# Kernel tuning notes

Hardware: AMD Instinct MI355X
Metric: run time of the kernel (lower is better)

## Reference

```python
import jax, jax.numpy as jnp
import numpy as np
from jax import lax

BN_EPS = 1e-4  # both BatchNorm2d (epsilon=0.0001) and BatchNorm1d (eps=0.0001)


def bin_act(x):
    # deterministic 1-bit activation: 2*round(clamp((x+1)/2,0,1)) - 1
    return 2.0 * jnp.round(jnp.clip((x + 1.0) * 0.5, 0.0, 1.0)) - 1.0


def bin_w(w):
    # H = 1.0: wb = (round(clamp((w+1)/2,0,1))*2 - 1) * 1.0  -> values in {-1,+1}
    return 2.0 * jnp.round(jnp.clip((w + 1.0) * 0.5, 0.0, 1.0)) - 1.0


def conv3x3(x, w, b):
    # NCHW input, OIHW weight, stride 1, padding 1 (SAME for 3x3)
    y = lax.conv_general_dilated(x, bin_w(w), (1, 1), ((1, 1), (1, 1)),
                                 dimension_numbers=('NCHW', 'OIHW', 'NCHW'))
    return y + b[None, :, None, None]


def maxpool2(x):
    return lax.reduce_window(x, -jnp.inf, lax.max, (1, 1, 2, 2), (1, 1, 2, 2), 'VALID')


def bn2d(x, g, b):
    # training-mode BatchNorm2d: batch stats over (N,H,W), biased variance
    m = jnp.mean(x, axis=(0, 2, 3), keepdims=True)
    v = jnp.mean(jnp.square(x - m), axis=(0, 2, 3), keepdims=True)
    return (x - m) * lax.rsqrt(v + BN_EPS) * g[None, :, None, None] + b[None, :, None, None]


def bn1d(x, g, b):
    m = jnp.mean(x, axis=0)
    v = jnp.mean(jnp.square(x - m), axis=0)
    return (x - m) * lax.rsqrt(v + BN_EPS) * g + b


def linear(x, w, b):
    return x @ bin_w(w).T + b


def setup_inputs() -> dict:
    key = jax.random.key(0)
    ks = jax.random.split(key, 16)
    d = {}
    d['x'] = jax.random.normal(ks[0], (256, 3, 32, 32), jnp.float32)
    conv_shapes = [(128, 3), (128, 128), (256, 128), (256, 256), (512, 256), (512, 512)]
    for i, (co, ci) in enumerate(conv_shapes, start=1):
        d[f'cw{i}'] = jax.random.normal(ks[i], (co, ci, 3, 3), jnp.float32)
        d[f'cb{i}'] = jax.random.normal(jax.random.fold_in(ks[i], 1), (co,), jnp.float32) * 0.01
        d[f'g{i}'] = jnp.ones((co,), jnp.float32)
        d[f'be{i}'] = jnp.zeros((co,), jnp.float32)
    fc_shapes = [(1024, 8192), (1024, 1024), (10, 1024)]
    for i, (fo, fi) in enumerate(fc_shapes, start=1):
        d[f'fw{i}'] = jax.random.normal(ks[6 + i], (fo, fi), jnp.float32)
        d[f'fb{i}'] = jax.random.normal(jax.random.fold_in(ks[6 + i], 1), (fo,), jnp.float32) * 0.01
        d[f'gf{i}'] = jnp.ones((fo,), jnp.float32)
        d[f'bef{i}'] = jnp.zeros((fo,), jnp.float32)
    return d


def reference(x, cw1, cb1, g1, be1, cw2, cb2, g2, be2, cw3, cb3, g3, be3,
              cw4, cb4, g4, be4, cw5, cb5, g5, be5, cw6, cb6, g6, be6,
              fw1, fb1, gf1, bef1, fw2, fb2, gf2, bef2, fw3, fb3, gf3, bef3):
    x = bin_act(bn2d(conv3x3(x, cw1, cb1), g1, be1))                 # [B,128,32,32]
    x = bin_act(bn2d(maxpool2(conv3x3(x, cw2, cb2)), g2, be2))       # [B,128,16,16]
    x = bin_act(bn2d(conv3x3(x, cw3, cb3), g3, be3))                 # [B,256,16,16]
    x = bin_act(bn2d(maxpool2(conv3x3(x, cw4, cb4)), g4, be4))       # [B,256,8,8]
    x = bin_act(bn2d(conv3x3(x, cw5, cb5), g5, be5))                 # [B,512,8,8]
    x = bin_act(bn2d(maxpool2(conv3x3(x, cw6, cb6)), g6, be6))       # [B,512,4,4]
    x = x.reshape(x.shape[0], -1)                                     # [B,8192]
    x = bin_act(bn1d(linear(x, fw1, fb1), gf1, bef1))                 # [B,1024]
    x = bin_act(bn1d(linear(x, fw2, fb2), gf2, bef2))                 # [B,1024]
    x = bn1d(linear(x, fw3, fb3), gf3, bef3)                          # [B,10]
    return x
```

## Files before the change

kernel.cpp:

```cpp
#include <hip/hip_runtime.h>

using u64 = unsigned long long;


__device__ __forceinline__ int bin01(float x) {
  float u = (x + 1.0f) * 0.5f;
  u = fminf(fmaxf(u, 0.0f), 1.0f);
  return rintf(u) != 0.0f;
}

__global__ void pack_conv_w(const float* __restrict__ w, u64* __restrict__ out,
                            int Cout, int Cin) {
  const int cqn = Cin >> 6;
  const int total = Cout * 9 * cqn;
  const int idx = blockIdx.x * 256 + threadIdx.x;
  if (idx >= total) return;
  int r = idx;
  const int q = r % cqn; r /= cqn;
  const int kx = r % 3; r /= 3;
  const int ky = r % 3;
  const int co = r / 3;
  u64 word = 0;
  for (int l = 0; l < 64; ++l) {
    const int ci = q * 64 + l;
    if (bin01(w[((size_t)(co * Cin + ci) * 3 + ky) * 3 + kx])) word |= (1ull << l);
  }
  out[idx] = word;
}

__global__ void pack_corr(const u64* __restrict__ W, int* __restrict__ CT) {
  const int idx = blockIdx.x * 256 + threadIdx.x;
  const int b1 = 1152, b2 = 3456, b3 = 5760, b4 = 10368, b5 = 14976;
  if (idx >= b5) return;
  int lo, woff, cq;
  if (idx < b1)      { lo = 0;  woff = 0;     cq = 2; }
  else if (idx < b2) { lo = b1; woff = 2304;  cq = 2; }
  else if (idx < b3) { lo = b2; woff = 6912;  cq = 4; }
  else if (idx < b4) { lo = b3; woff = 16128; cq = 4; }
  else               { lo = b4; woff = 34560; cq = 8; }
  const int rel = idx - lo;
  const int co = rel / 9, p = rel % 9;
  const int r = p / 3, c = p % 3;
  int corr = 0;
  for (int dy = 0; dy < 3; ++dy)
    for (int dx = 0; dx < 3; ++dx) {
      const bool inv = (r == 1 && dy == 0) || (r == 2 && dy == 2) ||
                       (c == 1 && dx == 0) || (c == 2 && dx == 2);
      if (inv) {
        const u64* wp = W + woff + ((size_t)(co * 9 + dy * 3 + dx)) * cq;
        for (int q = 0; q < cq; ++q) corr += __popcll(wp[q]);
      }
    }
  CT[idx] = corr;
}

__global__ void pack_fc_w(const float* __restrict__ w, u64* __restrict__ out,
                          int Fi, int Fo) {
  const int fiq = Fi >> 6;
  const int total = Fo * fiq;
  const int idx = blockIdx.x * 256 + threadIdx.x;
  if (idx >= total) return;
  const int q = idx % fiq, o = idx / fiq;
  u64 word = 0;
  for (int l = 0; l < 64; ++l)
    if (bin01(w[(size_t)o * Fi + q * 64 + l])) word |= (1ull << l);
  out[idx] = word;
}

__global__ void pack_fc1_w(const float* __restrict__ w, u64* __restrict__ out) {
  const int o = blockIdx.x;
  const int t = threadIdx.x;
  __shared__ float ls[8192];
  const float* wr = w + (size_t)o * 8192;
  for (int i = t; i < 8192; i += 256) ls[i] = wr[i];
  __syncthreads();
  if (t < 128) {
    const int q = t, cq = q & 7, hw = q >> 3;
    u64 word = 0;
    for (int l = 0; l < 64; ++l) {
      const int f = (cq * 64 + l) * 16 + hw;
      if (bin01(ls[f])) word |= (1ull << l);
    }
    out[(size_t)o * 128 + q] = word;
  }
}

__global__ void pack_w1f(const float* __restrict__ w1, float* __restrict__ w1f) {
  const int i = blockIdx.x * 256 + threadIdx.x;
  if (i < 3456) w1f[i] = bin01(w1[i]) ? 1.0f : -1.0f;
}

__device__ __forceinline__ void stage_image(const float* __restrict__ x, int n,
                                            float* __restrict__ xs, int nthreads,
                                            int t) {
  for (int idx = t; idx < 3 * 34 * 34; idx += nthreads) {
    const int ci = idx / 1156, rem = idx % 1156;
    const int hy = rem / 34, wx = rem % 34;
    float v = 0.0f;
    if (hy >= 1 && hy <= 32 && wx >= 1 && wx <= 32)
      v = x[(size_t)n * 3072 + ci * 1024 + (hy - 1) * 32 + (wx - 1)];
    xs[idx] = v;
  }
}

template <int PASS>
__global__ void conv1_eval(const float* __restrict__ x,
                           const float* __restrict__ w1f,
                           const float* __restrict__ cb,
                           const float* __restrict__ st,
                           float* __restrict__ BL) {
  const int blk = blockIdx.x;
  const int n = blk >> 2, q = blk & 3;
  const int t = threadIdx.x;
  __shared__ float xs[3 * 34 * 34];
  __shared__ float yl[256 * 8];
  __shared__ float rl[2 * 8 * 8];
  stage_image(x, n, xs, 256, t);
  __syncthreads();
  const int hw = q * 256 + t;
  const int h = hw >> 5, w = hw & 31;
  float win[27];
#pragma unroll
  for (int k = 0; k < 27; ++k) {
    const int ci = k / 9, dy = (k % 9) / 3, dx = k % 3;
    win[k] = xs[ci * 1156 + (h + dy) * 34 + (w + dx)];
  }
  for (int cc = 0; cc < 16; ++cc) {
    float y8[8];
#pragma unroll
    for (int j8 = 0; j8 < 8; ++j8) {
      const int c = cc * 8 + j8;
      const float* wp = w1f + c * 27;
      float acc = 0.0f;
#pragma unroll
      for (int k = 0; k < 27; ++k) acc = fmaf(wp[k], win[k], acc);
      float y = acc + cb[c];
      if (PASS) { const float d = y - st[2 * c]; y = d * d; }
      y8[j8] = y;
    }
    __syncthreads();
#pragma unroll
    for (int j8 = 0; j8 < 8; ++j8) yl[t * 8 + j8] = y8[j8];
    __syncthreads();
    if (t < 128) {
      const int L = t >> 6, j = (t >> 3) & 7, c8 = t & 7;
      float r = yl[(L * 128 + j) * 8 + c8];
      for (int i = 1; i < 16; ++i) r += yl[(L * 128 + i * 8 + j) * 8 + c8];
      rl[(L * 8 + c8) * 8 + j] = r;
    }
    __syncthreads();
    if (t < 16) {
      const int L = t >> 3, c8 = t & 7;
      const float* p = rl + (L * 8 + c8) * 8;
      const float s =
          ((p[0] + p[1]) + (p[2] + p[3])) + ((p[4] + p[5]) + (p[6] + p[7]));
      BL[((size_t)(n * 8) + (q * 2 + L)) * 128 + (cc * 8 + c8)] = s;
    }
  }
}

__global__ void conv1_comb2(const float* __restrict__ BL, float* __restrict__ st,
                            int pass) {
  const int t = threadIdx.x;
  const int lane = t & 63;
  const int wid = t >> 6;
  const int c = blockIdx.x * 32 + wid * 8 + (lane & 7);
  const int leaf = lane >> 3;
  const float* base = BL + (size_t)leaf * 128 + c;
  float S = 0.0f;
#pragma unroll 4
  for (int n = 0; n < 256; ++n) {
    const float v = base[(size_t)n * 1024];
    const float a = v + __shfl_xor(v, 8);
    const float b = a + __shfl_xor(a, 16);
    const float Ln = b + __shfl_xor(b, 32);
    S = (n == 0) ? Ln : (S + Ln);
  }
  if (leaf == 0) {
    if (pass == 0) st[2 * c] = S / 262144.0f;
    else           st[2 * c + 1] = 1.0f / sqrtf(S / 262144.0f + 1e-4f);
  }
}

__global__ void conv1_binz(const float* __restrict__ x,
                           const float* __restrict__ w1f,
                           const float* __restrict__ cb,
                           const float* __restrict__ st,
                           const float* __restrict__ g,
                           const float* __restrict__ be,
                           u64* __restrict__ out) {
  const int blk = blockIdx.x;
  const int n = blk >> 2, q = blk & 3;
  const int t = threadIdx.x;
  __shared__ float xs[3 * 34 * 34];
  stage_image(x, n, xs, 256, t);
  __syncthreads();
  const int hw = q * 256 + t;
  const int h = hw >> 5, w = hw & 31;
  float win[27];
#pragma unroll
  for (int k = 0; k < 27; ++k) {
    const int ci = k / 9, dy = (k % 9) / 3, dx = k % 3;
    win[k] = xs[ci * 1156 + (h + dy) * 34 + (w + dx)];
  }
  u64 m0 = 0, m1 = 0;
  for (int c = 0; c < 128; ++c) {
    const float* wp = w1f + c * 27;
    float acc = 0.0f;
#pragma unroll
    for (int k = 0; k < 27; ++k) acc = fmaf(wp[k], win[k], acc);
    const float y = acc + cb[c];
    const float tv = ((y - st[2 * c]) * st[2 * c + 1]) * g[c] + be[c];
    const u64 bit = (u64)bin01(tv);
    if (c < 64) m0 |= bit << c;
    else        m1 |= bit << (c - 64);
  }
  u64* dst = out + ((size_t)(n * 1024 + hw)) * 2;
  dst[0] = m0;
  dst[1] = m1;
}

template <int CQ, int H>
__device__ __forceinline__ void zero_halo(u64* __restrict__ xs, int t) {
  constexpr int HP = H + 2;
  constexpr int HALO = 2 * HP * CQ + 2 * H * CQ;
  for (int j = t; j < HALO; j += 256) {
    int widx;
    if (j < HP * CQ) widx = j;
    else if (j < 2 * HP * CQ) widx = (H + 1) * HP * CQ + (j - HP * CQ);
    else {
      const int r = j - 2 * HP * CQ;
      const int row = (r / (2 * CQ)) + 1;
      const int s = r & (2 * CQ - 1);
      const int col = (s < CQ) ? 0 : (HP - 1);
      widx = (row * HP + col) * CQ + (s & (CQ - 1));
    }
    xs[widx] = 0;
  }
}

template <int CQ, int POOL, int H, int COUT, int NCPB>
__launch_bounds__(256, 3)
__global__ void conv_bin_halo(const u64* __restrict__ xin, const u64* __restrict__ wpk,
                              const int* __restrict__ ct, short* __restrict__ pre) {
  constexpr int OH = H / POOL;
  constexpr int PLANE = OH * OH;
  constexpr int G = 256 / PLANE;
  constexpr int NE = POOL * POOL;
  constexpr int HP = H + 2;
  constexpr int NWP = HP * HP * CQ;
  constexpr int QC = (CQ > 4) ? 4 : CQ;
  constexpr int NQC = CQ / QC;
  constexpr int IW = H * H * CQ;
  constexpr int VEC = IW / 256;
  const int n = blockIdx.x;
  const int t = threadIdx.x;
  __shared__ __align__(16) u64 xs[NWP];
  const u64* src = xin + (size_t)n * IW;
  {
    const int i0 = t * VEC;
    const int q0 = i0 & (CQ - 1);
    const int w0 = (i0 / CQ) & (H - 1);
    const int h0 = i0 / (CQ * H);
    const int dst0 = ((h0 + 1) * HP + (w0 + 1)) * CQ + q0;
    if constexpr (VEC >= 2) {
      ulonglong2 tmp[VEC / 2];
#pragma unroll
      for (int v = 0; v < VEC / 2; ++v)
        tmp[v] = *reinterpret_cast<const ulonglong2*>(&src[i0 + 2 * v]);
      zero_halo<CQ, H>(xs, t);
#pragma unroll
      for (int v = 0; v < VEC / 2; ++v)
        *reinterpret_cast<ulonglong2*>(&xs[dst0 + 2 * v]) = tmp[v];
    } else {
      const u64 tv = src[i0];
      zero_halo<CQ, H>(xs, t);
      xs[dst0] = tv;
    }
  }
  __syncthreads();
  int cosub;
  if constexpr (PLANE >= 64) cosub = __builtin_amdgcn_readfirstlane(t / PLANE);
  else cosub = t / PLANE;
  const int pos = t % PLANE;
  const int oh = pos / OH, ow = pos % OH;

  int cbase[NE];
#pragma unroll
  for (int py = 0; py < POOL; ++py)
#pragma unroll
    for (int px = 0; px < POOL; ++px)
      cbase[py * POOL + px] = ((oh * POOL + py) * HP + (ow * POOL + px)) * CQ;

  int pc[NCPB][NE];
#pragma unroll
  for (int cc = 0; cc < NCPB; ++cc)
#pragma unroll
    for (int e = 0; e < NE; ++e) pc[cc][e] = 0;

#pragma unroll
  for (int qc = 0; qc < NQC; ++qc) {
#pragma unroll
    for (int k = 0; k < 9; ++k) {
      const int dy = k / 3, dx = k % 3;
      const int koff = (dy * HP + dx) * CQ + qc * QC;
      u64 cw[NE][QC];
#pragma unroll
      for (int e = 0; e < NE; ++e) {
        const u64* cp = &xs[cbase[e] + koff];
#pragma unroll
        for (int q = 0; q < QC; ++q) cw[e][q] = cp[q];
      }
#pragma unroll
      for (int cc = 0; cc < NCPB; ++cc) {
        const int co = (blockIdx.y * NCPB + cc) * G + cosub;
        const u64* wp = wpk + ((size_t)co * 9 + k) * CQ + qc * QC;
        u64 w[QC];
#pragma unroll
        for (int q = 0; q < QC; ++q) w[q] = wp[q];
#pragma unroll
        for (int e = 0; e < NE; ++e) {
          int acc = pc[cc][e];
#pragma unroll
          for (int q = 0; q < QC; ++q) acc += __popcll(cw[e][q] ^ w[q]);
          pc[cc][e] = acc;
        }
      }
    }
  }

  int vcnt[NE];
#pragma unroll
  for (int py = 0; py < POOL; ++py) {
#pragma unroll
    for (int px = 0; px < POOL; ++px) {
      int cvn = 0;
#pragma unroll
      for (int dy = 0; dy < 3; ++dy)
#pragma unroll
        for (int dx = 0; dx < 3; ++dx) {
          const int hh = oh * POOL + py + dy - 1, ww = ow * POOL + px + dx - 1;
          cvn += (((unsigned)hh < (unsigned)H) && ((unsigned)ww < (unsigned)H)) ? 1 : 0;
        }
      vcnt[py * POOL + px] = cvn;
    }
  }
  int cofs[NE];
#pragma unroll
  for (int py = 0; py < POOL; ++py)
#pragma unroll
    for (int px = 0; px < POOL; ++px) {
      const int chh = oh * POOL + py, cww = ow * POOL + px;
      const int rr = (chh == 0) ? 1 : ((chh == H - 1) ? 2 : 0);
      const int cl = (cww == 0) ? 1 : ((cww == H - 1) ? 2 : 0);
      cofs[py * POOL + px] = rr * 3 + cl;
    }
#pragma unroll
  for (int cc = 0; cc < NCPB; ++cc) {
    const int co = (blockIdx.y * NCPB + cc) * G + cosub;
    const int* ctp = ct + co * 9;
    int best = -1000000;
#pragma unroll
    for (int e = 0; e < NE; ++e) {
      const int dot = vcnt[e] * (CQ * 64) - 2 * (pc[cc][e] - ctp[cofs[e]]);
      best = dot > best ? dot : best;
    }
    pre[((size_t)(n * COUT + co) * OH + oh) * OH + ow] = (short)best;
  }
}

template <int CQ, int POOL, int H, int COUT, int NCPB>
__launch_bounds__(256, 4)
__global__ void conv_bin_pred(const u64* __restrict__ xin, const u64* __restrict__ wpk,
                              short* __restrict__ pre) {
  constexpr int OH = H / POOL;
  constexpr int PLANE = OH * OH;
  constexpr int G = 256 / PLANE;
  constexpr int NE = POOL * POOL;
  constexpr int NW_ = H * H * CQ;
  constexpr int QC = (CQ > 4) ? 4 : CQ;
  constexpr int NQC = CQ / QC;
  const int n = blockIdx.x;
  const int t = threadIdx.x;
  __shared__ u64 xs[NW_];
  const u64* src = xin + (size_t)n * NW_;
  for (int i = t; i < NW_; i += 256) xs[i] = src[i];
  __syncthreads();
  const int cosub = t / PLANE;
  const int pos = t % PLANE;
  const int oh = pos / OH, ow = pos % OH;

  int pc[NCPB][NE];
#pragma unroll
  for (int cc = 0; cc < NCPB; ++cc)
#pragma unroll
    for (int e = 0; e < NE; ++e) pc[cc][e] = 0;

#pragma unroll
  for (int qc = 0; qc < NQC; ++qc) {
#pragma unroll
    for (int k = 0; k < 9; ++k) {
      const int dy = k / 3, dx = k % 3;
      u64 cw[NE][QC];
      bool cv[NE];
#pragma unroll
      for (int py = 0; py < POOL; ++py) {
#pragma unroll
        for (int px = 0; px < POOL; ++px) {
          const int hh = oh * POOL + py + dy - 1;
          const int ww = ow * POOL + px + dx - 1;
          const bool v = ((unsigned)hh < (unsigned)H) && ((unsigned)ww < (unsigned)H);
          const int e = py * POOL + px;
          cv[e] = v;
          const int base = v ? ((hh * H + ww) * CQ + qc * QC) : 0;
#pragma unroll
          for (int q = 0; q < QC; ++q) cw[e][q] = xs[base + q];
        }
      }
#pragma unroll
      for (int cc = 0; cc < NCPB; ++cc) {
        const int co = (blockIdx.y * NCPB + cc) * G + cosub;
        const u64* wp = wpk + ((size_t)co * 9 + k) * CQ + qc * QC;
        u64 w[QC];
#pragma unroll
        for (int q = 0; q < QC; ++q) w[q] = wp[q];
#pragma unroll
        for (int e = 0; e < NE; ++e) {
          int tp = 0;
#pragma unroll
          for (int q = 0; q < QC; ++q) tp += __popcll(cw[e][q] ^ w[q]);
          pc[cc][e] += cv[e] ? tp : 0;
        }
      }
    }
  }

  int vcnt[NE];
#pragma unroll
  for (int py = 0; py < POOL; ++py) {
#pragma unroll
    for (int px = 0; px < POOL; ++px) {
      int cvn = 0;
#pragma unroll
      for (int dy = 0; dy < 3; ++dy)
#pragma unroll
        for (int dx = 0; dx < 3; ++dx) {
          const int hh = oh * POOL + py + dy - 1, ww = ow * POOL + px + dx - 1;
          cvn += (((unsigned)hh < (unsigned)H) && ((unsigned)ww < (unsigned)H)) ? 1 : 0;
        }
      vcnt[py * POOL + px] = cvn;
    }
  }
#pragma unroll
  for (int cc = 0; cc < NCPB; ++cc) {
    const int co = (blockIdx.y * NCPB + cc) * G + cosub;
    int best = -1000000;
#pragma unroll
    for (int e = 0; e < NE; ++e) {
      const int dot = vcnt[e] * (CQ * 64) - 2 * pc[cc][e];
      best = dot > best ? dot : best;
    }
    pre[((size_t)(n * COUT + co) * OH + oh) * OH + ow] = (short)best;
  }
}

template <int PASS>
__device__ __forceinline__ float acc8(const short* __restrict__ p, float b, float m,
                                      int start, int len) {
  float r[8];
#pragma unroll
  for (int j = 0; j < 8; ++j) {
    float y = (float)p[start + j] + b;
    if (PASS) { const float d = y - m; y = d * d; }
    r[j] = y;
  }
  for (int i = 8; i < len; i += 8) {
#pragma unroll
    for (int j = 0; j < 8; ++j) {
      float y = (float)p[start + i + j] + b;
      if (PASS) { const float d = y - m; y = d * d; }
      r[j] += y;
    }
  }
  return ((r[0] + r[1]) + (r[2] + r[3])) + ((r[4] + r[5]) + (r[6] + r[7]));
}

template <int PASS>
__device__ __forceinline__ float np_sum_hw(const short* __restrict__ p, float b,
                                           float m, int HW) {
  if (HW == 256) return acc8<PASS>(p, b, m, 0, 128) + acc8<PASS>(p, b, m, 128, 128);
  return acc8<PASS>(p, b, m, 0, HW);
}

template <int HW>
__global__ void conv_stats(const short* __restrict__ pre, const float* __restrict__ cb,
                           float* __restrict__ st, int Cout) {
  const int c = blockIdx.x;
  const int n = threadIdx.x;
  const float b = cb[c];
  const short* p = pre + ((size_t)n * Cout + c) * HW;
  __shared__ float ls[256];
  ls[n] = np_sum_hw<0>(p, b, 0.0f, HW);
  __syncthreads();
  __shared__ float ms;
  if (n == 0) {
    float S = ls[0];
    for (int i = 1; i < 256; ++i) S += ls[i];
    ms = S / (float)(256 * HW);
  }
  __syncthreads();
  const float m = ms;
  __syncthreads();
  ls[n] = np_sum_hw<1>(p, b, m, HW);
  __syncthreads();
  if (n == 0) {
    float S = ls[0];
    for (int i = 1; i < 256; ++i) S += ls[i];
    const float v = S / (float)(256 * HW);
    st[2 * c] = m;
    st[2 * c + 1] = 1.0f / sqrtf(v + 1e-4f);
  }
}

__global__ void bin2d(const short* __restrict__ pre, const float* __restrict__ st,
                      const float* __restrict__ cb, const float* __restrict__ g,
                      const float* __restrict__ be, u64* __restrict__ out,
                      int Cout, int OH) {
  const int CQ = Cout >> 6;
  const int HW = OH * OH;
  const int widx = blockIdx.x * 256 + threadIdx.x;
  const int hw = widx % HW;
  const int r = widx / HW;
  const int cq = r % CQ;
  const int n = r / CQ;
  const short* p = pre + ((size_t)(n * Cout + cq * 64)) * HW + hw;
  u64 mask = 0;
  for (int c = 0; c < 64; ++c) {
    const int ch = cq * 64 + c;
    const float val = (float)p[(size_t)c * HW] + cb[ch];
    const float tv = ((val - st[2 * ch]) * st[2 * ch + 1]) * g[ch] + be[ch];
    mask |= ((u64)bin01(tv)) << c;
  }
  out[((size_t)n * HW + hw) * CQ + cq] = mask;
}

__global__ void transpose_act(const u64* __restrict__ a, u64* __restrict__ at) {
  const int widx = blockIdx.x * 256 + threadIdx.x;
  const int n = widx >> 7, q = widx & 127;
  at[(size_t)q * 256 + n] = a[widx];
}

__global__ void fc_layer_t(const u64* __restrict__ at, const u64* __restrict__ wpk,
                           short* __restrict__ pre) {
  const int o = blockIdx.x;
  const int n = threadIdx.x;
  const u64* wp = wpk + (size_t)o * 128;
  int pc = 0;
#pragma unroll 8
  for (int q = 0; q < 128; ++q) pc += __popcll(at[(size_t)q * 256 + n] ^ wp[q]);
  pre[(size_t)n * 1024 + o] = (short)(8192 - 2 * pc);
}

__global__ void fc_layer(const u64* __restrict__ xin, const u64* __restrict__ wpk,
                         short* __restrict__ pre, int FiQ, int Fo) {
  const int o = blockIdx.x;
  const int n = threadIdx.x;
  const u64* xp = xin + (size_t)n * FiQ;
  const u64* wp = wpk + (size_t)o * FiQ;
  int pc = 0;
  for (int q = 0; q < FiQ; ++q) pc += __popcll(xp[q] ^ wp[q]);
  pre[(size_t)n * Fo + o] = (short)(FiQ * 64 - 2 * pc);
}

__global__ void fc_stats(const short* __restrict__ pre, const float* __restrict__ fb,
                         float* __restrict__ st, int Fo) {
  const int o = blockIdx.x * blockDim.x + threadIdx.x;
  if (o >= Fo) return;
  const float b = fb[o];
  float S = (float)pre[o] + b;
#pragma unroll 8
  for (int n = 1; n < 256; ++n) S += (float)pre[(size_t)n * Fo + o] + b;
  const float m = S / 256.0f;
  float d0 = (float)pre[o] + b - m;
  float V = d0 * d0;
#pragma unroll 8
  for (int n = 1; n < 256; ++n) {
    const float d = (float)pre[(size_t)n * Fo + o] + b - m;
    V += d * d;
  }
  st[2 * o] = m;
  st[2 * o + 1] = 1.0f / sqrtf(V / 256.0f + 1e-4f);
}

__global__ void fc_bin(const short* __restrict__ pre, const float* __restrict__ st,
                       const float* __restrict__ fb, const float* __restrict__ g,
                       const float* __restrict__ be, u64* __restrict__ out, int Fo) {
  const int gid = blockIdx.x * 4 + (threadIdx.x >> 6);
  const int lane = threadIdx.x & 63;
  const int OQ = Fo >> 6;
  const int oq = gid % OQ, n = gid / OQ;
  const int o = oq * 64 + lane;
  const float val = (float)pre[(size_t)n * Fo + o] + fb[o];
  const float tv = ((val - st[2 * o]) * st[2 * o + 1]) * g[o] + be[o];
  const u64 mask = __ballot(bin01(tv));
  if (lane == 0) out[(size_t)n * OQ + oq] = mask;
}

__global__ void fc_out(const short* __restrict__ pre, const float* __restrict__ st,
                       const float* __restrict__ fb, const float* __restrict__ g,
                       const float* __restrict__ be, float* __restrict__ out) {
  const int i = blockIdx.x * 256 + threadIdx.x;
  if (i >= 2560) return;
  const int o = i % 10;
  const float val = (float)pre[i] + fb[o];
  out[i] = ((val - st[2 * o]) * st[2 * o + 1]) * g[o] + be[o];
}

extern "C" void kernel_launch(void* const* d_in, const int* in_sizes, int n_in,
                              void* d_out, int out_size, void* d_ws, size_t ws_size,
                              hipStream_t stream) {
  if (n_in < 37) return;
  const float* x = (const float*)d_in[0];
  const float *cw1 = (const float*)d_in[1],  *cb1 = (const float*)d_in[2],  *g1 = (const float*)d_in[3],  *be1 = (const float*)d_in[4];
  const float *cw2 = (const float*)d_in[5],  *cb2 = (const float*)d_in[6],  *g2 = (const float*)d_in[7],  *be2 = (const float*)d_in[8];
  const float *cw3 = (const float*)d_in[9],  *cb3 = (const float*)d_in[10], *g3 = (const float*)d_in[11], *be3 = (const float*)d_in[12];
  const float *cw4 = (const float*)d_in[13], *cb4 = (const float*)d_in[14], *g4 = (const float*)d_in[15], *be4 = (const float*)d_in[16];
  const float *cw5 = (const float*)d_in[17], *cb5 = (const float*)d_in[18], *g5 = (const float*)d_in[19], *be5 = (const float*)d_in[20];
  const float *cw6 = (const float*)d_in[21], *cb6 = (const float*)d_in[22], *g6 = (const float*)d_in[23], *be6 = (const float*)d_in[24];
  const float *fw1 = (const float*)d_in[25], *fb1 = (const float*)d_in[26], *gf1 = (const float*)d_in[27], *bef1 = (const float*)d_in[28];
  const float *fw2 = (const float*)d_in[29], *fb2 = (const float*)d_in[30], *gf2 = (const float*)d_in[31], *bef2 = (const float*)d_in[32];
  const float *fw3 = (const float*)d_in[33], *fb3 = (const float*)d_in[34], *gf3 = (const float*)d_in[35], *bef3 = (const float*)d_in[36];
  float* out = (float*)d_out;

  char* ws = (char*)d_ws;
  if (ws_size < 46137344) return;
  float* ST = (float*)ws;
  float* W1F = (float*)(ws + 32768);
  float* BL = (float*)(ws + 65536);
  u64* W = (u64*)(ws + 1179648);
  u64* A = (u64*)(ws + 2981888);
  int* CT = (int*)(ws + 12222464);
  short* PRE = (short*)(ws + 12582912);
  u64* AT6 = (u64*)(ws + 33554432);
  const int S1 = 0, S2 = 256, S3 = 512, S4 = 1024, S5 = 1536, S6 = 2560;
  const int SF1 = 3584, SF2 = 5632, SF3 = 7680;
  const size_t WC2 = 0, WC3 = 2304, WC4 = 6912, WC5 = 16128, WC6 = 34560;
  const size_t WF1 = 71424, WF2 = 202496, WF3 = 218880;
  const size_t A1 = 0, A2 = 524288, A3 = 655360, A4 = 917504, A5 = 983040;
  const size_t A6 = 1114112, AF1 = 1146880, AF2 = 1150976;
  const int CT2 = 0, CT3 = 1152, CT4 = 3456, CT5 = 5760;

  pack_w1f<<<14, 256, 0, stream>>>(cw1, W1F);
  pack_conv_w<<<9, 256, 0, stream>>>(cw2, W + WC2, 128, 128);
  pack_conv_w<<<18, 256, 0, stream>>>(cw3, W + WC3, 256, 128);
  pack_conv_w<<<36, 256, 0, stream>>>(cw4, W + WC4, 256, 256);
  pack_conv_w<<<72, 256, 0, stream>>>(cw5, W + WC5, 512, 256);
  pack_conv_w<<<144, 256, 0, stream>>>(cw6, W + WC6, 512, 512);
  pack_corr<<<59, 256, 0, stream>>>(W, CT);
  pack_fc1_w<<<1024, 256, 0, stream>>>(fw1, W + WF1);
  pack_fc_w<<<64, 256, 0, stream>>>(fw2, W + WF2, 1024, 1024);
  pack_fc_w<<<1, 256, 0, stream>>>(fw3, W + WF3, 1024, 10);

  conv1_eval<0><<<1024, 256, 0, stream>>>(x, W1F, cb1, ST + S1, BL);
  conv1_comb2<<<4, 256, 0, stream>>>(BL, ST + S1, 0);
  conv1_eval<1><<<1024, 256, 0, stream>>>(x, W1F, cb1, ST + S1, BL);
  conv1_comb2<<<4, 256, 0, stream>>>(BL, ST + S1, 1);
  conv1_binz<<<1024, 256, 0, stream>>>(x, W1F, cb1, ST + S1, g1, be1, A + A1);

  conv_bin_halo<2, 2, 32, 128, 8><<<dim3(256, 16), 256, 0, stream>>>(A + A1, W + WC2, CT + CT2, PRE);
  conv_stats<256><<<128, 256, 0, stream>>>(PRE, cb2, ST + S2, 128);
  bin2d<<<512, 256, 0, stream>>>(PRE, ST + S2, cb2, g2, be2, A + A2, 128, 16);

  conv_bin_halo<2, 1, 16, 256, 8><<<dim3(256, 32), 256, 0, stream>>>(A + A2, W + WC3, CT + CT3, PRE);
  conv_stats<256><<<256, 256, 0, stream>>>(PRE, cb3, ST + S3, 256);
  bin2d<<<1024, 256, 0, stream>>>(PRE, ST + S3, cb3, g3, be3, A + A3, 256, 16);

  conv_bin_halo<4, 2, 16, 256, 4><<<dim3(256, 16), 256, 0, stream>>>(A + A3, W + WC4, CT + CT4, PRE);
  conv_stats<64><<<256, 256, 0, stream>>>(PRE, cb4, ST + S4, 256);
  bin2d<<<256, 256, 0, stream>>>(PRE, ST + S4, cb4, g4, be4, A + A4, 256, 8);

  conv_bin_halo<4, 1, 8, 512, 8><<<dim3(256, 16), 256, 0, stream>>>(A + A4, W + WC5, CT + CT5, PRE);
  conv_stats<64><<<512, 256, 0, stream>>>(PRE, cb5, ST + S5, 512);
  bin2d<<<512, 256, 0, stream>>>(PRE, ST + S5, cb5, g5, be5, A + A5, 512, 8);

  conv_bin_pred<8, 2, 8, 512, 4><<<dim3(256, 8), 256, 0, stream>>>(A + A5, W + WC6, PRE);
  conv_stats<16><<<512, 256, 0, stream>>>(PRE, cb6, ST + S6, 512);
  bin2d<<<128, 256, 0, stream>>>(PRE, ST + S6, cb6, g6, be6, A + A6, 512, 4);

  transpose_act<<<128, 256, 0, stream>>>(A + A6, AT6);
  fc_layer_t<<<1024, 256, 0, stream>>>(AT6, W + WF1, PRE);
  fc_stats<<<16, 64, 0, stream>>>(PRE, fb1, ST + SF1, 1024);
  fc_bin<<<1024, 256, 0, stream>>>(PRE, ST + SF1, fb1, gf1, bef1, A + AF1, 1024);

  fc_layer<<<1024, 256, 0, stream>>>(A + AF1, W + WF2, PRE, 16, 1024);
  fc_stats<<<16, 64, 0, stream>>>(PRE, fb2, ST + SF2, 1024);
  fc_bin<<<1024, 256, 0, stream>>>(PRE, ST + SF2, fb2, gf2, bef2, A + AF2, 1024);

  fc_layer<<<10, 256, 0, stream>>>(A + AF2, W + WF3, PRE, 16, 10);
  fc_stats<<<1, 64, 0, stream>>>(PRE, fb3, ST + SF3, 10);
  fc_out<<<10, 256, 0, stream>>>(PRE, ST + SF3, fb3, gf3, bef3, out);
}
```

Before: 1.070 ms.

## Stage conv weights in LDS for packing, vectorize loads, fuse final FC layer

Conv weight packing now uses one block per output channel. Each block stages that channel's weights into shared memory with float4 loads and packs from there, instead of each thread doing strided global reads. The fc1 packing staging loop and the BN stats accumulation also switch to vectorized loads (float4 and 8-wide short). The last FC layer, its batch stats and its output normalization are merged into one single-block kernel, removing two launches. In exchange, the fused kernel computes its stats with only 10 threads in a serial loop, and the vector loads assume suitable alignment.

```diff
diff --git a/kernel.cpp b/kernel.cpp
--- a/kernel.cpp
+++ b/kernel.cpp
@@ -1,6 +1,7 @@
 #include <hip/hip_runtime.h>
 
 using u64 = unsigned long long;
+typedef __attribute__((ext_vector_type(8))) short vshort8;
 
 
 __device__ __forceinline__ int bin01(float x) {
@@ -9,23 +10,26 @@
   return rintf(u) != 0.0f;
 }
 
-__global__ void pack_conv_w(const float* __restrict__ w, u64* __restrict__ out,
-                            int Cout, int Cin) {
+__global__ void pack_conv_w2(const float* __restrict__ w, u64* __restrict__ out,
+                             int Cin) {
+  const int co = blockIdx.x;
+  const int t = threadIdx.x;
+  const int nf = Cin * 9;
+  __shared__ float ls[4608];
+  const float* wr = w + (size_t)co * nf;
+  const int nf4 = nf >> 2;
+  for (int i = t; i < nf4; i += 256)
+    *reinterpret_cast<float4*>(&ls[i * 4]) =
+        *reinterpret_cast<const float4*>(&wr[i * 4]);
+  __syncthreads();
   const int cqn = Cin >> 6;
-  const int total = Cout * 9 * cqn;
-  const int idx = blockIdx.x * 256 + threadIdx.x;
-  if (idx >= total) return;
-  int r = idx;
-  const int q = r % cqn; r /= cqn;
-  const int kx = r % 3; r /= 3;
-  const int ky = r % 3;
-  const int co = r / 3;
-  u64 word = 0;
-  for (int l = 0; l < 64; ++l) {
-    const int ci = q * 64 + l;
-    if (bin01(w[((size_t)(co * Cin + ci) * 3 + ky) * 3 + kx])) word |= (1ull << l);
-  }
-  out[idx] = word;
+  for (int idx = t; idx < 9 * cqn; idx += 256) {
+    const int q = idx % cqn, k = idx / cqn;
+    u64 word = 0;
+    for (int l = 0; l < 64; ++l)
+      if (bin01(ls[(q * 64 + l) * 9 + k])) word |= (1ull << l);
+    out[(size_t)co * 9 * cqn + idx] = word;
+  }
 }
 
 __global__ void pack_corr(const u64* __restrict__ W, int* __restrict__ CT) {
@@ -72,7 +76,9 @@
   const int t = threadIdx.x;
   __shared__ float ls[8192];
   const float* wr = w + (size_t)o * 8192;
-  for (int i = t; i < 8192; i += 256) ls[i] = wr[i];
+  for (int i = t; i < 2048; i += 256)
+    *reinterpret_cast<float4*>(&ls[i * 4]) =
+        *reinterpret_cast<const float4*>(&wr[i * 4]);
   __syncthreads();
   if (t < 128) {
     const int q = t, cq = q & 7, hw = q >> 3;
@@ -468,16 +474,18 @@
 __device__ __forceinline__ float acc8(const short* __restrict__ p, float b, float m,
                                       int start, int len) {
   float r[8];
+  const vshort8 v0 = *reinterpret_cast<const vshort8*>(&p[start]);
 #pragma unroll
   for (int j = 0; j < 8; ++j) {
-    float y = (float)p[start + j] + b;
+    float y = (float)v0[j] + b;
     if (PASS) { const float d = y - m; y = d * d; }
     r[j] = y;
   }
   for (int i = 8; i < len; i += 8) {
+    const vshort8 vi = *reinterpret_cast<const vshort8*>(&p[start + i]);
 #pragma unroll
     for (int j = 0; j < 8; ++j) {
-      float y = (float)p[start + i + j] + b;
+      float y = (float)vi[j] + b;
       if (PASS) { const float d = y - m; y = d * d; }
       r[j] += y;
     }
@@ -606,14 +614,43 @@
   if (lane == 0) out[(size_t)n * OQ + oq] = mask;
 }
 
-__global__ void fc_out(const short* __restrict__ pre, const float* __restrict__ st,
-                       const float* __restrict__ fb, const float* __restrict__ g,
-                       const float* __restrict__ be, float* __restrict__ out) {
-  const int i = blockIdx.x * 256 + threadIdx.x;
-  if (i >= 2560) return;
-  const int o = i % 10;
-  const float val = (float)pre[i] + fb[o];
-  out[i] = ((val - st[2 * o]) * st[2 * o + 1]) * g[o] + be[o];
+__global__ void fc3_fused(const u64* __restrict__ xin, const u64* __restrict__ wpk,
+                          const float* __restrict__ fb, const float* __restrict__ g,
+                          const float* __restrict__ be, float* __restrict__ out) {
+  const int n = threadIdx.x;
+  __shared__ short lpre[2560];
+  __shared__ float st[20];
+  u64 xw[16];
+  const u64* xp = xin + (size_t)n * 16;
+#pragma unroll
+  for (int q = 0; q < 16; ++q) xw[q] = xp[q];
+  for (int o = 0; o < 10; ++o) {
+    const u64* wp = wpk + (size_t)o * 16;
+    int pc = 0;
+#pragma unroll
+    for (int q = 0; q < 16; ++q) pc += __popcll(xw[q] ^ wp[q]);
+    lpre[n * 10 + o] = (short)(1024 - 2 * pc);
+  }
+  __syncthreads();
+  if (n < 10) {
+    const float b = fb[n];
+    float S = (float)lpre[n] + b;
+    for (int i = 1; i < 256; ++i) S += (float)lpre[i * 10 + n] + b;
+    const float m = S / 256.0f;
+    float d0 = (float)lpre[n] + b - m;
+    float V = d0 * d0;
+    for (int i = 1; i < 256; ++i) {
+      const float d = (float)lpre[i * 10 + n] + b - m;
+      V += d * d;
+    }
+    st[2 * n] = m;
+    st[2 * n + 1] = 1.0f / sqrtf(V / 256.0f + 1e-4f);
+  }
+  __syncthreads();
+  for (int o = 0; o < 10; ++o) {
+    const float val = (float)lpre[n * 10 + o] + fb[o];
+    out[n * 10 + o] = ((val - st[2 * o]) * st[2 * o + 1]) * g[o] + be[o];
+  }
 }
 
 extern "C" void kernel_launch(void* const* d_in, const int* in_sizes, int n_in,
@@ -643,7 +680,7 @@
   short* PRE = (short*)(ws + 12582912);
   u64* AT6 = (u64*)(ws + 33554432);
   const int S1 = 0, S2 = 256, S3 = 512, S4 = 1024, S5 = 1536, S6 = 2560;
-  const int SF1 = 3584, SF2 = 5632, SF3 = 7680;
+  const int SF1 = 3584, SF2 = 5632;
   const size_t WC2 = 0, WC3 = 2304, WC4 = 6912, WC5 = 16128, WC6 = 34560;
   const size_t WF1 = 71424, WF2 = 202496, WF3 = 218880;
   const size_t A1 = 0, A2 = 524288, A3 = 655360, A4 = 917504, A5 = 983040;
@@ -651,11 +688,11 @@
   const int CT2 = 0, CT3 = 1152, CT4 = 3456, CT5 = 5760;
 
   pack_w1f<<<14, 256, 0, stream>>>(cw1, W1F);
-  pack_conv_w<<<9, 256, 0, stream>>>(cw2, W + WC2, 128, 128);
-  pack_conv_w<<<18, 256, 0, stream>>>(cw3, W + WC3, 256, 128);
-  pack_conv_w<<<36, 256, 0, stream>>>(cw4, W + WC4, 256, 256);
-  pack_conv_w<<<72, 256, 0, stream>>>(cw5, W + WC5, 512, 256);
-  pack_conv_w<<<144, 256, 0, stream>>>(cw6, W + WC6, 512, 512);
+  pack_conv_w2<<<128, 256, 0, stream>>>(cw2, W + WC2, 128);
+  pack_conv_w2<<<256, 256, 0, stream>>>(cw3, W + WC3, 128);
+  pack_conv_w2<<<256, 256, 0, stream>>>(cw4, W + WC4, 256);
+  pack_conv_w2<<<512, 256, 0, stream>>>(cw5, W + WC5, 256);
+  pack_conv_w2<<<512, 256, 0, stream>>>(cw6, W + WC6, 512);
   pack_corr<<<59, 256, 0, stream>>>(W, CT);
   pack_fc1_w<<<1024, 256, 0, stream>>>(fw1, W + WF1);
   pack_fc_w<<<64, 256, 0, stream>>>(fw2, W + WF2, 1024, 1024);
@@ -696,7 +733,5 @@
   fc_stats<<<16, 64, 0, stream>>>(PRE, fb2, ST + SF2, 1024);
   fc_bin<<<1024, 256, 0, stream>>>(PRE, ST + SF2, fb2, gf2, bef2, A + AF2, 1024);
 
-  fc_layer<<<10, 256, 0, stream>>>(A + AF2, W + WF3, PRE, 16, 10);
-  fc_stats<<<1, 64, 0, stream>>>(PRE, fb3, ST + SF3, 10);
-  fc_out<<<10, 256, 0, stream>>>(PRE, ST + SF3, fb3, gf3, bef3, out);
-}
+  fc3_fused<<<1, 256, 0, stream>>>(A + AF2, W + WF3, fb3, gf3, bef3, out);
+}
```

After: 1.158 ms. +8.2%, slower.
